# Kernel tuning notes

Measured on AMD Instinct MI355X. Metric: run time of the kernel, lower is better.

Reference implementation:

```python
import jax, jax.numpy as jnp
import numpy as np

B = 32768          # batch
SEQ, F = 128, 8    # input_seq_len_samples, num_features
D = SEQ * F        # flattened input dim = 1024
E = 16             # num_experts
H1 = 256           # expert hidden
H2 = H1 // 2       # 128
GH = 128           # gating hidden


def _init_linear(key, fan_in, shape_w, shape_b):
    # torch nn.Linear default: U(-1/sqrt(fan_in), 1/sqrt(fan_in))
    kw, kb = jax.random.split(key)
    lim = 1.0 / np.sqrt(fan_in)
    W = jax.random.uniform(kw, shape_w, jnp.float32, -lim, lim)
    b = jax.random.uniform(kb, shape_b, jnp.float32, -lim, lim)
    return W, b


def setup_inputs() -> dict:
    key = jax.random.key(0)
    ks = jax.random.split(key, 6)
    x = jax.random.normal(ks[0], (B, SEQ, F), jnp.float32)
    # stacked expert weights: [E, in, out] layout
    W1, b1 = _init_linear(ks[1], D, (E, D, H1), (E, H1))
    W2, b2 = _init_linear(ks[2], H1, (E, H1, H2), (E, H2))
    W3, b3 = _init_linear(ks[3], H2, (E, H2, 1), (E, 1))
    Wg1, bg1 = _init_linear(ks[4], D, (D, GH), (GH,))
    Wg2, bg2 = _init_linear(ks[5], GH, (GH, E), (E,))
    return {"x": x, "W1": W1, "b1": b1, "W2": W2, "b2": b2,
            "W3": W3, "b3": b3, "Wg1": Wg1, "bg1": bg1,
            "Wg2": Wg2, "bg2": bg2}


def reference(x, W1, b1, W2, b2, W3, b3, Wg1, bg1, Wg2, bg2):
    bsz = x.shape[0]
    flat_x = x.reshape(bsz, -1)                      # [B, D]
    # gating network
    g = jax.nn.relu(flat_x @ Wg1 + bg1)              # [B, GH]
    gating_logits = g @ Wg2 + bg2                    # [B, E]
    gating_weights = jax.nn.softmax(gating_logits, axis=1)
    # all experts as one batched GEMM stack
    h = jax.nn.relu(jnp.einsum('bd,edh->beh', flat_x, W1) + b1)   # [B,E,H1]
    h = jax.nn.relu(jnp.einsum('beh,ehk->bek', h, W2) + b2)       # [B,E,H2]
    expert_outputs = jnp.einsum('bek,eko->beo', h, W3) + b3       # [B,E,1]
    final_output = jnp.sum(gating_weights[:, :, None] * expert_outputs, axis=1)  # [B,1]
    return final_output, gating_weights
```

## Files before the change

### kernel.cpp

```cpp
#include <hip/hip_runtime.h>
#include <stdint.h>
#include <stddef.h>

typedef short bf16x8 __attribute__((ext_vector_type(8)));
typedef float f32x4 __attribute__((ext_vector_type(4)));

__device__ __forceinline__ unsigned short bf16rn(float f){
  unsigned int u = __builtin_bit_cast(unsigned int, f);
  u += 0x7fffu + ((u >> 16) & 1u);
  return (unsigned short)(u >> 16);
}

__device__ __forceinline__ void gll16(const void* gsrc, void* ldst){
  __builtin_amdgcn_global_load_lds((const __attribute__((address_space(1))) unsigned int*)gsrc,
                                   (__attribute__((address_space(3))) unsigned int*)ldst,
                                   16, 0, 0);
}

__device__ __forceinline__ void barfence(){
  asm volatile("" ::: "memory");
  __builtin_amdgcn_s_barrier();
  asm volatile("" ::: "memory");
}

__global__ __launch_bounds__(256) void k_cvt_x(const float* __restrict__ x,
                                               unsigned short* __restrict__ xb, long n){
  long i = ((long)blockIdx.x * blockDim.x + threadIdx.x) * 8;
  if (i >= n) return;
  const float4* p = (const float4*)(x + i);
  float4 a = p[0], b = p[1];
  union { unsigned short h[8]; uint4 u; } r;
  r.h[0]=bf16rn(a.x); r.h[1]=bf16rn(a.y); r.h[2]=bf16rn(a.z); r.h[3]=bf16rn(a.w);
  r.h[4]=bf16rn(b.x); r.h[5]=bf16rn(b.y); r.h[6]=bf16rn(b.z); r.h[7]=bf16rn(b.w);
  *(uint4*)(xb + i) = r.u;
}

__global__ __launch_bounds__(256) void k_cvt_w(const float* __restrict__ src,
                                               unsigned short* __restrict__ dst,
                                               int K, int N){
  __shared__ float t[32][33];
  int e = blockIdx.z, k0 = blockIdx.x * 32, n0 = blockIdx.y * 32;
  const float* s = src + (size_t)e * K * N;
  unsigned short* d = dst + (size_t)e * N * K;
  int tx = threadIdx.x, ty = threadIdx.y;
  #pragma unroll
  for (int j = 0; j < 4; j++)
    t[ty + j*8][tx] = s[(size_t)(k0 + ty + j*8) * N + n0 + tx];
  __syncthreads();
  #pragma unroll
  for (int j = 0; j < 4; j++){
    int n = ty + j*8;
    d[(size_t)(n0 + n) * K + k0 + tx] = bf16rn(t[tx][n]);
  }
}

__global__ __launch_bounds__(128) void k_gating(const unsigned short* __restrict__ xb,
                                                const unsigned short* __restrict__ wg1t,
                                                const float* __restrict__ bg1,
                                                const float* __restrict__ wg2,
                                                const float* __restrict__ bg2,
                                                float* __restrict__ gout, int chunk_base){
  __shared__ unsigned short As[32*64];
  __shared__ unsigned short Bs[128*64];
  __shared__ float gl[32][129];
  const int t = threadIdx.x, wid = t >> 6, l = t & 63;
  const int m0 = blockIdx.x * 32;
  const int jb = l & 7, rsub = l >> 3;
  f32x4 acc[2][4];
  #pragma unroll
  for (int i=0;i<2;i++)
    #pragma unroll
    for (int j=0;j<4;j++) acc[i][j] = (f32x4)0.f;

  for (int kt = 0; kt < 16; kt++){
    int k0 = kt * 64;
    #pragma unroll
    for (int i = 0; i < 2; i++){
      int idx = wid*2 + i; int row = idx*8 + rsub;
      gll16(xb + (size_t)(m0 + row)*1024 + k0 + ((jb ^ (row & 7)) << 3), As + idx*512);
    }
    #pragma unroll
    for (int i = 0; i < 8; i++){
      int idx = wid*8 + i; int row = idx*8 + rsub;
      gll16(wg1t + (size_t)row*1024 + k0 + ((jb ^ (row & 7)) << 3), Bs + idx*512);
    }
    __syncthreads();
    #pragma unroll
    for (int ks = 0; ks < 2; ks++){
      int blk = ks*4 + (l >> 4);
      bf16x8 a[2], b[4];
      #pragma unroll
      for (int fi = 0; fi < 2; fi++){
        int r = fi*16 + (l & 15);
        a[fi] = *(const bf16x8*)(As + r*64 + ((blk ^ (r & 7)) << 3));
      }
      #pragma unroll
      for (int fj = 0; fj < 4; fj++){
        int r = wid*64 + fj*16 + (l & 15);
        b[fj] = *(const bf16x8*)(Bs + r*64 + ((blk ^ (r & 7)) << 3));
      }
      #pragma unroll
      for (int fi = 0; fi < 2; fi++)
        #pragma unroll
        for (int fj = 0; fj < 4; fj++)
          acc[fi][fj] = __builtin_amdgcn_mfma_f32_16x16x32_bf16(a[fi], b[fj], acc[fi][fj], 0, 0, 0);
    }
    __syncthreads();
  }
  #pragma unroll
  for (int fi = 0; fi < 2; fi++)
    #pragma unroll
    for (int fj = 0; fj < 4; fj++){
      int c = wid*64 + fj*16 + (l & 15);
      float bv = bg1[c];
      #pragma unroll
      for (int r = 0; r < 4; r++){
        int row = fi*16 + (l >> 4)*4 + r;
        float v = acc[fi][fj][r] + bv;
        gl[row][c] = v > 0.f ? v : 0.f;
      }
    }
  __syncthreads();
  if (t < 32){
    float le[16];
    #pragma unroll
    for (int e = 0; e < 16; e++) le[e] = bg2[e];
    for (int k = 0; k < 128; k++){
      float g = gl[t][k];
      const float* w = wg2 + k*16;
      #pragma unroll
      for (int e = 0; e < 16; e++) le[e] += g * w[e];
    }
    float m = le[0];
    #pragma unroll
    for (int e = 1; e < 16; e++) m = fmaxf(m, le[e]);
    float s = 0.f;
    #pragma unroll
    for (int e = 0; e < 16; e++){ le[e] = __expf(le[e] - m); s += le[e]; }
    float inv = 1.f / s;
    float4* o = (float4*)(gout + (size_t)(chunk_base + m0 + t)*16);
    #pragma unroll
    for (int q = 0; q < 4; q++)
      o[q] = make_float4(le[4*q]*inv, le[4*q+1]*inv, le[4*q+2]*inv, le[4*q+3]*inv);
  }
}

template<int I0, int J0>
__device__ __forceinline__ void mfma_quad(const bf16x8 (&A)[4][2], const bf16x8 (&Bv)[2][2],
                                          f32x4 (&acc)[8][4]){
  #pragma unroll
  for (int fi = 0; fi < 4; ++fi)
    #pragma unroll
    for (int ks = 0; ks < 2; ++ks){
      acc[I0+fi][J0]   = __builtin_amdgcn_mfma_f32_16x16x32_bf16(A[fi][ks], Bv[0][ks], acc[I0+fi][J0],   0,0,0);
      acc[I0+fi][J0+1] = __builtin_amdgcn_mfma_f32_16x16x32_bf16(A[fi][ks], Bv[1][ks], acc[I0+fi][J0+1], 0,0,0);
    }
}

__global__ __launch_bounds__(512, 2) void k_fused(const unsigned short* __restrict__ xb,
                                                  const unsigned short* __restrict__ w1t,
                                                  const float* __restrict__ b1,
                                                  const unsigned short* __restrict__ w2t,
                                                  const float* __restrict__ b2,
                                                  const float* __restrict__ w3,
                                                  const float* __restrict__ b3,
                                                  float* __restrict__ outE,
                                                  int chunkB){
  extern __shared__ __align__(16) char smem[];
  const int t = threadIdx.x;
  const int wid = t >> 6, l = t & 63;
  const int wrow = wid >> 2, wcol = wid & 3;
  const int l3 = l >> 3, l7 = l & 7, l15 = l & 15, l4 = l >> 4;

  const int bid = blockIdx.x;
  const int slot = bid >> 3;
  const int e = (bid & 7)*2 + (slot & 1);
  const int mt = slot >> 1;
  const int m0 = mt * 256, n0 = e * 256;

  auto STAGE = [&](int isB, int p, int h, int kt){
    const unsigned short* gb = isB ? (w1t + (size_t)(n0 + h*128) * 1024)
                                   : (xb  + (size_t)(m0 + h*128) * 1024);
    char* dbase = smem + ((p << 16) | (isB << 15) | (h << 14));
    #pragma unroll
    for (int j = 0; j < 2; j++){
      int r = j*64 + wid*8 + l3;
      size_t src = (size_t)r * 1024 + (size_t)kt*64 + (size_t)((l7 ^ (r & 7)) << 3);
      gll16(gb + src, dbase + j*8192 + wid*1024);
    }
  };
  auto LDA = [&](int p, int qm, int fi, int ks) -> bf16x8 {
    int row = qm*64 + fi*16 + l15;
    int kb = (((ks << 2) | l4) ^ (row & 7)) << 4;
    return *(const bf16x8*)(smem + (p << 16) + (wrow << 14) + row*128 + kb);
  };
  auto LDB = [&](int p, int qn, int fj, int ks) -> bf16x8 {
    int row = (wcol & 1)*64 + qn*32 + fj*16 + l15;
    int kb = (((ks << 2) | l4) ^ (row & 7)) << 4;
    return *(const bf16x8*)(smem + (p << 16) + 32768 + ((wcol >> 1) << 14) + row*128 + kb);
  };

  f32x4 acc[8][4];
  #pragma unroll
  for (int i = 0; i < 8; i++)
    #pragma unroll
    for (int j = 0; j < 4; j++) acc[i][j] = (f32x4)0.f;

  bf16x8 a0[4][2], a1[4][2], b0[2][2], b1v[2][2];

  STAGE(0,0,0,0); STAGE(1,0,0,0); STAGE(0,0,1,0); STAGE(1,0,1,0);
  STAGE(1,1,0,1); STAGE(0,1,0,1);
  asm volatile("s_waitcnt vmcnt(4)" ::: "memory");
  barfence();

  for (int it = 0; it < 8; ++it){
    const int t0 = 2*it, k1 = t0 + 1;
    int c2 = t0 + 2, c3 = t0 + 3;
    if (c2 > 15) c2 = 14;
    if (c3 > 15) c3 = 14;

    #pragma unroll
    for (int fi = 0; fi < 4; ++fi){ a0[fi][0] = LDA(0,0,fi,0); a0[fi][1] = LDA(0,0,fi,1); }
    #pragma unroll
    for (int fj = 0; fj < 2; ++fj){ b0[fj][0] = LDB(0,0,fj,0); b0[fj][1] = LDB(0,0,fj,1); }
    STAGE(1,1,1,k1);
    barfence();
    __builtin_amdgcn_s_setprio(1);
    mfma_quad<0,0>(a0, b0, acc);
    __builtin_amdgcn_s_setprio(0);
    barfence();

    #pragma unroll
    for (int fj = 0; fj < 2; ++fj){ b1v[fj][0] = LDB(0,1,fj,0); b1v[fj][1] = LDB(0,1,fj,1); }
    STAGE(0,1,1,k1);
    barfence();
    __builtin_amdgcn_s_setprio(1);
    mfma_quad<0,2>(a0, b1v, acc);
    __builtin_amdgcn_s_setprio(0);
    barfence();

    #pragma unroll
    for (int fi = 0; fi < 4; ++fi){ a1[fi][0] = LDA(0,1,fi,0); a1[fi][1] = LDA(0,1,fi,1); }
    STAGE(1,0,0,c2);
    barfence();
    __builtin_amdgcn_s_setprio(1);
    mfma_quad<4,2>(a1, b1v, acc);
    __builtin_amdgcn_s_setprio(0);
    barfence();

    STAGE(0,0,0,c2);
    barfence();
    __builtin_amdgcn_s_setprio(1);
    mfma_quad<4,0>(a1, b0, acc);
    __builtin_amdgcn_s_setprio(0);
    asm volatile("s_waitcnt vmcnt(4)" ::: "memory");
    barfence();

    #pragma unroll
    for (int fi = 0; fi < 4; ++fi){ a0[fi][0] = LDA(1,0,fi,0); a0[fi][1] = LDA(1,0,fi,1); }
    #pragma unroll
    for (int fj = 0; fj < 2; ++fj){ b0[fj][0] = LDB(1,0,fj,0); b0[fj][1] = LDB(1,0,fj,1); }
    STAGE(1,0,1,c2);
    barfence();
    __builtin_amdgcn_s_setprio(1);
    mfma_quad<0,0>(a0, b0, acc);
    __builtin_amdgcn_s_setprio(0);
    barfence();

    #pragma unroll
    for (int fj = 0; fj < 2; ++fj){ b1v[fj][0] = LDB(1,1,fj,0); b1v[fj][1] = LDB(1,1,fj,1); }
    STAGE(0,0,1,c2);
    barfence();
    __builtin_amdgcn_s_setprio(1);
    mfma_quad<0,2>(a0, b1v, acc);
    __builtin_amdgcn_s_setprio(0);
    barfence();

    #pragma unroll
    for (int fi = 0; fi < 4; ++fi){ a1[fi][0] = LDA(1,1,fi,0); a1[fi][1] = LDA(1,1,fi,1); }
    STAGE(1,1,0,c3);
    barfence();
    __builtin_amdgcn_s_setprio(1);
    mfma_quad<4,2>(a1, b1v, acc);
    __builtin_amdgcn_s_setprio(0);
    barfence();

    STAGE(0,1,0,c3);
    barfence();
    __builtin_amdgcn_s_setprio(1);
    mfma_quad<4,0>(a1, b0, acc);
    __builtin_amdgcn_s_setprio(0);
    asm volatile("s_waitcnt vmcnt(4)" ::: "memory");
    barfence();
  }

  __syncthreads();

  {
    float bv[4];
    #pragma unroll
    for (int fj = 0; fj < 4; ++fj) bv[fj] = b1[e*256 + wcol*64 + fj*16 + l15];
    #pragma unroll
    for (int fi = 0; fi < 8; ++fi)
      #pragma unroll
      for (int fj = 0; fj < 4; ++fj){
        const int col = wcol*64 + fj*16 + l15;
        #pragma unroll
        for (int r = 0; r < 4; ++r){
          const int row = wrow*128 + fi*16 + l4*4 + r;
          float v = acc[fi][fj][r] + bv[fj];
          v = v > 0.f ? v : 0.f;
          *(unsigned short*)(smem + row*512 + (((col >> 3) ^ (row & 7)) << 4) + ((col & 7) << 1)) = bf16rn(v);
        }
      }
  }

  const unsigned short* w2e = w2t + (size_t)e*(128*256);
  auto STAGE_W2 = [&](int c, int q){
    char* dbase = smem + 131072 + q*16384;
    #pragma unroll
    for (int j = 0; j < 2; j++){
      int r = j*64 + wid*8 + l3;
      size_t src = (size_t)r*256 + (size_t)c*64 + (size_t)((l7 ^ (r & 7)) << 3);
      gll16(w2e + src, dbase + j*8192 + wid*1024);
    }
  };
  STAGE_W2(0, 0);
  __syncthreads();

  const int wr2 = wid >> 1, wc2 = wid & 1;
  f32x4 acc2[4][4];
  #pragma unroll
  for (int i = 0; i < 4; i++)
    #pragma unroll
    for (int j = 0; j < 4; j++) acc2[i][j] = (f32x4)0.f;

  float w3v[4], b2v[4];
  #pragma unroll
  for (int fj = 0; fj < 4; ++fj){
    int c = wc2*64 + fj*16 + l15;
    w3v[fj] = w3[e*128 + c];
    b2v[fj] = b2[e*128 + c];
  }

  for (int c = 0; c < 4; ++c){
    if (c < 3) STAGE_W2(c+1, (c+1)&1);
    bf16x8 a2[4][2], bb[4][2];
    #pragma unroll
    for (int fi = 0; fi < 4; ++fi)
      #pragma unroll
      for (int ks = 0; ks < 2; ++ks){
        int row = wr2*64 + fi*16 + l15;
        int sl = (c*8 + ks*4 + l4) ^ (row & 7);
        a2[fi][ks] = *(const bf16x8*)(smem + row*512 + (sl << 4));
      }
    #pragma unroll
    for (int fj = 0; fj < 4; ++fj)
      #pragma unroll
      for (int ks = 0; ks < 2; ++ks){
        int n = wc2*64 + fj*16 + l15;
        int sl = (ks*4 + l4) ^ (n & 7);
        bb[fj][ks] = *(const bf16x8*)(smem + 131072 + (c&1)*16384 + n*128 + (sl << 4));
      }
    __builtin_amdgcn_s_setprio(1);
    #pragma unroll
    for (int fi = 0; fi < 4; ++fi)
      #pragma unroll
      for (int fj = 0; fj < 4; ++fj)
        #pragma unroll
        for (int ks = 0; ks < 2; ++ks)
          acc2[fi][fj] = __builtin_amdgcn_mfma_f32_16x16x32_bf16(a2[fi][ks], bb[fj][ks], acc2[fi][fj], 0, 0, 0);
    __builtin_amdgcn_s_setprio(0);
    __syncthreads();
  }

  float* red = (float*)(smem + 131072);
  #pragma unroll
  for (int fi = 0; fi < 4; ++fi)
    #pragma unroll
    for (int r = 0; r < 4; ++r){
      float s = 0.f;
      #pragma unroll
      for (int fj = 0; fj < 4; ++fj){
        float v = acc2[fi][fj][r] + b2v[fj];
        v = v > 0.f ? v : 0.f;
        s += v * w3v[fj];
      }
      s += __shfl_xor(s, 1); s += __shfl_xor(s, 2);
      s += __shfl_xor(s, 4); s += __shfl_xor(s, 8);
      if (l15 == 0){
        int row = wr2*64 + fi*16 + l4*4 + r;
        red[row*2 + wc2] = s;
      }
    }
  __syncthreads();
  if (t < 256)
    outE[(size_t)e*chunkB + m0 + t] = red[t*2 + 0] + red[t*2 + 1] + b3[e];
}

__global__ __launch_bounds__(256) void k_stage2b(const float* __restrict__ outE,
                                                 float* __restrict__ dout,
                                                 int chunk_base, int chunkB, int Btot){
  int row = blockIdx.x*256 + threadIdx.x;
  int rowg = chunk_base + row;
  const float* g = dout + Btot + (size_t)rowg*16;
  float s = 0.f;
  #pragma unroll
  for (int e = 0; e < 16; e++) s += g[e] * outE[(size_t)e*chunkB + row];
  dout[rowg] = s;
}

extern "C" void kernel_launch(void* const* d_in, const int* in_sizes, int n_in,
                              void* d_out, int out_size, void* d_ws, size_t ws_size,
                              hipStream_t stream){
  const float* x   = (const float*)d_in[0];
  const float* W1  = (const float*)d_in[1];
  const float* b1  = (const float*)d_in[2];
  const float* W2  = (const float*)d_in[3];
  const float* b2  = (const float*)d_in[4];
  const float* W3  = (const float*)d_in[5];
  const float* b3  = (const float*)d_in[6];
  const float* Wg1 = (const float*)d_in[7];
  const float* bg1 = (const float*)d_in[8];
  const float* Wg2 = (const float*)d_in[9];
  const float* bg2 = (const float*)d_in[10];
  float* out = (float*)d_out;

  const int B = in_sizes[0] / 1024;

  char* ws = (char*)d_ws;
  size_t off = 0;
  auto alloc = [&](size_t bytes){ size_t p = off; off = (off + bytes + 255) & ~(size_t)255; return p; };
  size_t o_w1t  = alloc((size_t)16*256*1024*2);
  size_t o_w2t  = alloc((size_t)16*128*256*2);
  size_t o_wg1t = alloc((size_t)128*1024*2);
  size_t fixed = off;

  const int cands[6] = {1, 2, 4, 8, 16, 32};
  int nc = 32;
  for (int i = 0; i < 6; i++){
    size_t cB = (size_t)B / cands[i];
    if (fixed + cB*2112 + 4096 <= ws_size){ nc = cands[i]; break; }
  }
  int chunkB = B / nc;

  size_t o_xb = alloc((size_t)chunkB*1024*2);
  size_t o_oe = alloc((size_t)chunkB*16*4);

  unsigned short* w1t  = (unsigned short*)(ws + o_w1t);
  unsigned short* w2t  = (unsigned short*)(ws + o_w2t);
  unsigned short* wg1t = (unsigned short*)(ws + o_wg1t);
  unsigned short* xb   = (unsigned short*)(ws + o_xb);
  float*          oE   = (float*)(ws + o_oe);

  hipFuncSetAttribute(reinterpret_cast<const void*>(k_fused),
                      hipFuncAttributeMaxDynamicSharedMemorySize, 163840);

  k_cvt_w<<<dim3(32, 8, 16), dim3(32, 8), 0, stream>>>(W1, w1t, 1024, 256);
  k_cvt_w<<<dim3(8, 4, 16),  dim3(32, 8), 0, stream>>>(W2, w2t, 256, 128);
  k_cvt_w<<<dim3(32, 4, 1),  dim3(32, 8), 0, stream>>>(Wg1, wg1t, 1024, 128);

  for (int c = 0; c < nc; c++){
    int cb = c * chunkB;
    k_cvt_x<<<chunkB/2, 256, 0, stream>>>(x + (size_t)cb*1024, xb, (long)chunkB*1024);
    k_gating<<<chunkB/32, 128, 0, stream>>>(xb, wg1t, bg1, Wg2, bg2, out + B, cb);
    k_fused<<<chunkB/16, 512, 163840, stream>>>(xb, w1t, b1, w2t, b2, W3, b3, oE, chunkB);
    k_stage2b<<<chunkB/256, 256, 0, stream>>>(oE, out, cb, chunkB, B);
  }
}
```

Baseline: 366.4 us.

## Shrink fused expert block to 128-row tiles with 256 threads and triple-buffered K32 pipeline

Restructures the fused expert MLP kernel from 512-thread blocks covering a 256x256 tile to 256-thread blocks covering a 128x256 tile. The K loop now steps 32 at a time through a simple three-stage LDS ring with a single barrier per step, replacing the hand-interleaved two-stage ping-pong schedule. The second GEMM is re-tiled so each wave owns 32 output columns. Shared memory drops to 80KB, which may allow more resident blocks per CU, but each block reuses the W1 tile over fewer rows, so W1 is reloaded more often.

```diff
diff --git a/kernel.cpp b/kernel.cpp
--- a/kernel.cpp
+++ b/kernel.cpp
@@ -145,19 +145,7 @@
   }
 }
 
-template<int I0, int J0>
-__device__ __forceinline__ void mfma_quad(const bf16x8 (&A)[4][2], const bf16x8 (&Bv)[2][2],
-                                          f32x4 (&acc)[8][4]){
-  #pragma unroll
-  for (int fi = 0; fi < 4; ++fi)
-    #pragma unroll
-    for (int ks = 0; ks < 2; ++ks){
-      acc[I0+fi][J0]   = __builtin_amdgcn_mfma_f32_16x16x32_bf16(A[fi][ks], Bv[0][ks], acc[I0+fi][J0],   0,0,0);
-      acc[I0+fi][J0+1] = __builtin_amdgcn_mfma_f32_16x16x32_bf16(A[fi][ks], Bv[1][ks], acc[I0+fi][J0+1], 0,0,0);
-    }
-}
-
-__global__ __launch_bounds__(512, 2) void k_fused(const unsigned short* __restrict__ xb,
+__global__ __launch_bounds__(256, 2) void k_fused(const unsigned short* __restrict__ xb,
                                                   const unsigned short* __restrict__ w1t,
                                                   const float* __restrict__ b1,
                                                   const unsigned short* __restrict__ w2t,
@@ -169,35 +157,41 @@
   extern __shared__ __align__(16) char smem[];
   const int t = threadIdx.x;
   const int wid = t >> 6, l = t & 63;
-  const int wrow = wid >> 2, wcol = wid & 3;
-  const int l3 = l >> 3, l7 = l & 7, l15 = l & 15, l4 = l >> 4;
+  const int l15 = l & 15, l4 = l >> 4;
+  const int l2 = l & 3, lr = l >> 2;
 
   const int bid = blockIdx.x;
   const int slot = bid >> 3;
   const int e = (bid & 7)*2 + (slot & 1);
   const int mt = slot >> 1;
-  const int m0 = mt * 256, n0 = e * 256;
-
-  auto STAGE = [&](int isB, int p, int h, int kt){
-    const unsigned short* gb = isB ? (w1t + (size_t)(n0 + h*128) * 1024)
-                                   : (xb  + (size_t)(m0 + h*128) * 1024);
-    char* dbase = smem + ((p << 16) | (isB << 15) | (h << 14));
+  const int m0 = mt * 128, n0 = e * 256;
+
+  auto swz4 = [](int r){ return (r & 3) ^ ((r >> 2) & 3); };
+
+  auto STAGE = [&](int p, int kt){
+    char* ab = smem + p*24576;
     #pragma unroll
     for (int j = 0; j < 2; j++){
-      int r = j*64 + wid*8 + l3;
-      size_t src = (size_t)r * 1024 + (size_t)kt*64 + (size_t)((l7 ^ (r & 7)) << 3);
-      gll16(gb + src, dbase + j*8192 + wid*1024);
+      int idx = wid*2 + j;
+      int r = idx*16 + lr;
+      gll16(xb + (size_t)(m0 + r)*1024 + kt*32 + ((l2 ^ swz4(r)) << 3),
+            ab + idx*1024);
+    }
+    #pragma unroll
+    for (int j = 0; j < 4; j++){
+      int idx = wid*4 + j;
+      int r = idx*16 + lr;
+      gll16(w1t + (size_t)(n0 + r)*1024 + kt*32 + ((l2 ^ swz4(r)) << 3),
+            ab + 8192 + idx*1024);
     }
   };
-  auto LDA = [&](int p, int qm, int fi, int ks) -> bf16x8 {
-    int row = qm*64 + fi*16 + l15;
-    int kb = (((ks << 2) | l4) ^ (row & 7)) << 4;
-    return *(const bf16x8*)(smem + (p << 16) + (wrow << 14) + row*128 + kb);
+  auto LDA = [&](int p, int fi) -> bf16x8 {
+    int r = fi*16 + l15;
+    return *(const bf16x8*)(smem + p*24576 + r*64 + ((l4 ^ swz4(r)) << 4));
   };
-  auto LDB = [&](int p, int qn, int fj, int ks) -> bf16x8 {
-    int row = (wcol & 1)*64 + qn*32 + fj*16 + l15;
-    int kb = (((ks << 2) | l4) ^ (row & 7)) << 4;
-    return *(const bf16x8*)(smem + (p << 16) + 32768 + ((wcol >> 1) << 14) + row*128 + kb);
+  auto LDB = [&](int p, int fj) -> bf16x8 {
+    int n = wid*64 + fj*16 + l15;
+    return *(const bf16x8*)(smem + p*24576 + 8192 + n*64 + ((l4 ^ swz4(n)) << 4));
   };
 
   f32x4 acc[8][4];
@@ -206,91 +200,29 @@
     #pragma unroll
     for (int j = 0; j < 4; j++) acc[i][j] = (f32x4)0.f;
 
-  bf16x8 a0[4][2], a1[4][2], b0[2][2], b1v[2][2];
-
-  STAGE(0,0,0,0); STAGE(1,0,0,0); STAGE(0,0,1,0); STAGE(1,0,1,0);
-  STAGE(1,1,0,1); STAGE(0,1,0,1);
-  asm volatile("s_waitcnt vmcnt(4)" ::: "memory");
+  STAGE(0, 0); STAGE(1, 1);
+  asm volatile("s_waitcnt vmcnt(6)" ::: "memory");
   barfence();
 
-  for (int it = 0; it < 8; ++it){
-    const int t0 = 2*it, k1 = t0 + 1;
-    int c2 = t0 + 2, c3 = t0 + 3;
-    if (c2 > 15) c2 = 14;
-    if (c3 > 15) c3 = 14;
-
-    #pragma unroll
-    for (int fi = 0; fi < 4; ++fi){ a0[fi][0] = LDA(0,0,fi,0); a0[fi][1] = LDA(0,0,fi,1); }
-    #pragma unroll
-    for (int fj = 0; fj < 2; ++fj){ b0[fj][0] = LDB(0,0,fj,0); b0[fj][1] = LDB(0,0,fj,1); }
-    STAGE(1,1,1,k1);
-    barfence();
+  for (int kt = 0; kt < 32; ++kt){
+    int nx = kt + 2; if (nx > 31) nx = 31;
+    STAGE((kt + 2) % 3, nx);
+
+    bf16x8 av[8], bv[4];
+    #pragma unroll
+    for (int fi = 0; fi < 8; ++fi) av[fi] = LDA(kt % 3, fi);
+    #pragma unroll
+    for (int fj = 0; fj < 4; ++fj) bv[fj] = LDB(kt % 3, fj);
+
     __builtin_amdgcn_s_setprio(1);
-    mfma_quad<0,0>(a0, b0, acc);
+    #pragma unroll
+    for (int fi = 0; fi < 8; ++fi)
+      #pragma unroll
+      for (int fj = 0; fj < 4; ++fj)
+        acc[fi][fj] = __builtin_amdgcn_mfma_f32_16x16x32_bf16(av[fi], bv[fj], acc[fi][fj], 0, 0, 0);
     __builtin_amdgcn_s_setprio(0);
-    barfence();
-
-    #pragma unroll
-    for (int fj = 0; fj < 2; ++fj){ b1v[fj][0] = LDB(0,1,fj,0); b1v[fj][1] = LDB(0,1,fj,1); }
-    STAGE(0,1,1,k1);
-    barfence();
-    __builtin_amdgcn_s_setprio(1);
-    mfma_quad<0,2>(a0, b1v, acc);
-    __builtin_amdgcn_s_setprio(0);
-    barfence();
-
-    #pragma unroll
-    for (int fi = 0; fi < 4; ++fi){ a1[fi][0] = LDA(0,1,fi,0); a1[fi][1] = LDA(0,1,fi,1); }
-    STAGE(1,0,0,c2);
-    barfence();
-    __builtin_amdgcn_s_setprio(1);
-    mfma_quad<4,2>(a1, b1v, acc);
-    __builtin_amdgcn_s_setprio(0);
-    barfence();
-
-    STAGE(0,0,0,c2);
-    barfence();
-    __builtin_amdgcn_s_setprio(1);
-    mfma_quad<4,0>(a1, b0, acc);
-    __builtin_amdgcn_s_setprio(0);
-    asm volatile("s_waitcnt vmcnt(4)" ::: "memory");
-    barfence();
-
-    #pragma unroll
-    for (int fi = 0; fi < 4; ++fi){ a0[fi][0] = LDA(1,0,fi,0); a0[fi][1] = LDA(1,0,fi,1); }
-    #pragma unroll
-    for (int fj = 0; fj < 2; ++fj){ b0[fj][0] = LDB(1,0,fj,0); b0[fj][1] = LDB(1,0,fj,1); }
-    STAGE(1,0,1,c2);
-    barfence();
-    __builtin_amdgcn_s_setprio(1);
-    mfma_quad<0,0>(a0, b0, acc);
-    __builtin_amdgcn_s_setprio(0);
-    barfence();
-
-    #pragma unroll
-    for (int fj = 0; fj < 2; ++fj){ b1v[fj][0] = LDB(1,1,fj,0); b1v[fj][1] = LDB(1,1,fj,1); }
-    STAGE(0,0,1,c2);
-    barfence();
-    __builtin_amdgcn_s_setprio(1);
-    mfma_quad<0,2>(a0, b1v, acc);
-    __builtin_amdgcn_s_setprio(0);
-    barfence();
-
-    #pragma unroll
-    for (int fi = 0; fi < 4; ++fi){ a1[fi][0] = LDA(1,1,fi,0); a1[fi][1] = LDA(1,1,fi,1); }
-    STAGE(1,1,0,c3);
-    barfence();
-    __builtin_amdgcn_s_setprio(1);
-    mfma_quad<4,2>(a1, b1v, acc);
-    __builtin_amdgcn_s_setprio(0);
-    barfence();
-
-    STAGE(0,1,0,c3);
-    barfence();
-    __builtin_amdgcn_s_setprio(1);
-    mfma_quad<4,0>(a1, b0, acc);
-    __builtin_amdgcn_s_setprio(0);
-    asm volatile("s_waitcnt vmcnt(4)" ::: "memory");
+
+    asm volatile("s_waitcnt vmcnt(6)" ::: "memory");
     barfence();
   }
 
@@ -299,15 +231,15 @@
   {
     float bv[4];
     #pragma unroll
-    for (int fj = 0; fj < 4; ++fj) bv[fj] = b1[e*256 + wcol*64 + fj*16 + l15];
+    for (int fj = 0; fj < 4; ++fj) bv[fj] = b1[e*256 + wid*64 + fj*16 + l15];
     #pragma unroll
     for (int fi = 0; fi < 8; ++fi)
       #pragma unroll
       for (int fj = 0; fj < 4; ++fj){
-        const int col = wcol*64 + fj*16 + l15;
+        const int col = wid*64 + fj*16 + l15;
         #pragma unroll
         for (int r = 0; r < 4; ++r){
-          const int row = wrow*128 + fi*16 + l4*4 + r;
+          const int row = fi*16 + l4*4 + r;
           float v = acc[fi][fj][r] + bv[fj];
           v = v > 0.f ? v : 0.f;
           *(unsigned short*)(smem + row*512 + (((col >> 3) ^ (row & 7)) << 4) + ((col & 7) << 1)) = bf16rn(v);
@@ -317,71 +249,64 @@
 
   const unsigned short* w2e = w2t + (size_t)e*(128*256);
   auto STAGE_W2 = [&](int c, int q){
-    char* dbase = smem + 131072 + q*16384;
+    char* dbase = smem + 65536 + q*8192;
     #pragma unroll
     for (int j = 0; j < 2; j++){
-      int r = j*64 + wid*8 + l3;
-      size_t src = (size_t)r*256 + (size_t)c*64 + (size_t)((l7 ^ (r & 7)) << 3);
-      gll16(w2e + src, dbase + j*8192 + wid*1024);
+      int idx = wid*2 + j;
+      int r = idx*16 + lr;
+      gll16(w2e + (size_t)r*256 + c*32 + ((l2 ^ swz4(r)) << 3), dbase + idx*1024);
     }
   };
   STAGE_W2(0, 0);
   __syncthreads();
 
-  const int wr2 = wid >> 1, wc2 = wid & 1;
-  f32x4 acc2[4][4];
-  #pragma unroll
-  for (int i = 0; i < 4; i++)
-    #pragma unroll
-    for (int j = 0; j < 4; j++) acc2[i][j] = (f32x4)0.f;
-
-  float w3v[4], b2v[4];
-  #pragma unroll
-  for (int fj = 0; fj < 4; ++fj){
-    int c = wc2*64 + fj*16 + l15;
-    w3v[fj] = w3[e*128 + c];
-    b2v[fj] = b2[e*128 + c];
-  }
-
-  for (int c = 0; c < 4; ++c){
-    if (c < 3) STAGE_W2(c+1, (c+1)&1);
-    bf16x8 a2[4][2], bb[4][2];
-    #pragma unroll
-    for (int fi = 0; fi < 4; ++fi)
-      #pragma unroll
-      for (int ks = 0; ks < 2; ++ks){
-        int row = wr2*64 + fi*16 + l15;
-        int sl = (c*8 + ks*4 + l4) ^ (row & 7);
-        a2[fi][ks] = *(const bf16x8*)(smem + row*512 + (sl << 4));
-      }
-    #pragma unroll
-    for (int fj = 0; fj < 4; ++fj)
-      #pragma unroll
-      for (int ks = 0; ks < 2; ++ks){
-        int n = wc2*64 + fj*16 + l15;
-        int sl = (ks*4 + l4) ^ (n & 7);
-        bb[fj][ks] = *(const bf16x8*)(smem + 131072 + (c&1)*16384 + n*128 + (sl << 4));
-      }
+  f32x4 acc2[8][2];
+  #pragma unroll
+  for (int i = 0; i < 8; i++)
+    #pragma unroll
+    for (int j = 0; j < 2; j++) acc2[i][j] = (f32x4)0.f;
+
+  float w3v[2], b2v[2];
+  #pragma unroll
+  for (int fj = 0; fj < 2; ++fj){
+    int n = wid*32 + fj*16 + l15;
+    w3v[fj] = w3[e*128 + n];
+    b2v[fj] = b2[e*128 + n];
+  }
+
+  #pragma unroll
+  for (int c = 0; c < 8; ++c){
+    if (c < 7) STAGE_W2(c+1, (c+1)&1);
+    bf16x8 ah[8], bw[2];
+    #pragma unroll
+    for (int fi = 0; fi < 8; ++fi){
+      int row = fi*16 + l15;
+      int sl = (c*4 + l4) ^ (row & 7);
+      ah[fi] = *(const bf16x8*)(smem + row*512 + (sl << 4));
+    }
+    #pragma unroll
+    for (int fj = 0; fj < 2; ++fj){
+      int n = wid*32 + fj*16 + l15;
+      bw[fj] = *(const bf16x8*)(smem + 65536 + (c&1)*8192 + n*64 + ((l4 ^ swz4(n)) << 4));
+    }
     __builtin_amdgcn_s_setprio(1);
     #pragma unroll
-    for (int fi = 0; fi < 4; ++fi)
-      #pragma unroll
-      for (int fj = 0; fj < 4; ++fj)
-        #pragma unroll
-        for (int ks = 0; ks < 2; ++ks)
-          acc2[fi][fj] = __builtin_amdgcn_mfma_f32_16x16x32_bf16(a2[fi][ks], bb[fj][ks], acc2[fi][fj], 0, 0, 0);
+    for (int fi = 0; fi < 8; ++fi)
+      #pragma unroll
+      for (int fj = 0; fj < 2; ++fj)
+        acc2[fi][fj] = __builtin_amdgcn_mfma_f32_16x16x32_bf16(ah[fi], bw[fj], acc2[fi][fj], 0, 0, 0);
     __builtin_amdgcn_s_setprio(0);
     __syncthreads();
   }
 
-  float* red = (float*)(smem + 131072);
-  #pragma unroll
-  for (int fi = 0; fi < 4; ++fi)
+  float* red = (float*)(smem + 65536);
+  #pragma unroll
+  for (int fi = 0; fi < 8; ++fi)
     #pragma unroll
     for (int r = 0; r < 4; ++r){
       float s = 0.f;
       #pragma unroll
-      for (int fj = 0; fj < 4; ++fj){
+      for (int fj = 0; fj < 2; ++fj){
         float v = acc2[fi][fj][r] + b2v[fj];
         v = v > 0.f ? v : 0.f;
         s += v * w3v[fj];
@@ -389,13 +314,13 @@
       s += __shfl_xor(s, 1); s += __shfl_xor(s, 2);
       s += __shfl_xor(s, 4); s += __shfl_xor(s, 8);
       if (l15 == 0){
-        int row = wr2*64 + fi*16 + l4*4 + r;
-        red[row*2 + wc2] = s;
-      }
-    }
-  __syncthreads();
-  if (t < 256)
-    outE[(size_t)e*chunkB + m0 + t] = red[t*2 + 0] + red[t*2 + 1] + b3[e];
+        int row = fi*16 + l4*4 + r;
+        red[row*4 + wid] = s;
+      }
+    }
+  __syncthreads();
+  if (t < 128)
+    outE[(size_t)e*chunkB + m0 + t] = red[t*4+0] + red[t*4+1] + red[t*4+2] + red[t*4+3] + b3[e];
 }
 
 __global__ __launch_bounds__(256) void k_stage2b(const float* __restrict__ outE,
@@ -454,7 +379,7 @@
   float*          oE   = (float*)(ws + o_oe);
 
   hipFuncSetAttribute(reinterpret_cast<const void*>(k_fused),
-                      hipFuncAttributeMaxDynamicSharedMemorySize, 163840);
+                      hipFuncAttributeMaxDynamicSharedMemorySize, 81920);
 
   k_cvt_w<<<dim3(32, 8, 16), dim3(32, 8), 0, stream>>>(W1, w1t, 1024, 256);
   k_cvt_w<<<dim3(8, 4, 16),  dim3(32, 8), 0, stream>>>(W2, w2t, 256, 128);
@@ -464,7 +389,7 @@
     int cb = c * chunkB;
     k_cvt_x<<<chunkB/2, 256, 0, stream>>>(x + (size_t)cb*1024, xb, (long)chunkB*1024);
     k_gating<<<chunkB/32, 128, 0, stream>>>(xb, wg1t, bg1, Wg2, bg2, out + B, cb);
-    k_fused<<<chunkB/16, 512, 163840, stream>>>(xb, w1t, b1, w2t, b2, W3, b3, oE, chunkB);
+    k_fused<<<(chunkB/128)*16, 256, 81920, stream>>>(xb, w1t, b1, w2t, b2, W3, b3, oE, chunkB);
     k_stage2b<<<chunkB/256, 256, 0, stream>>>(oE, out, cb, chunkB, B);
   }
 }
```

Result: slower. 401.9 us (+9.7%).
